# Performance work log

Measured on AMD Instinct MI355X. Metric: run time of the kernel, lower is better.

## Reference

```python
import jax, jax.numpy as jnp
import numpy as np

HEADS = 12
EPS = 1e-5

def setup_inputs() -> dict:
    key = jax.random.key(0)
    ks = jax.random.split(key, 24)
    B, T, H = 128, 128, 768
    RIN, RH, NT = 512, 512, 10
    s = 0.02
    inp = {
        'slot_vector': jax.random.normal(ks[0], (B, H), jnp.float32),
        'utt_vectors': jax.random.normal(ks[1], (B, T, H), jnp.float32),
        'Wq': jax.random.normal(ks[2], (H, H), jnp.float32) * s,
        'bq': jnp.zeros((H,), jnp.float32),
        'Wk': jax.random.normal(ks[3], (H, H), jnp.float32) * s,
        'bk': jnp.zeros((H,), jnp.float32),
        'Wv': jax.random.normal(ks[4], (H, H), jnp.float32) * s,
        'bv': jnp.zeros((H,), jnp.float32),
        'Wo': jax.random.normal(ks[5], (H, H), jnp.float32) * s,
        'bo': jnp.zeros((H,), jnp.float32),
        'W_in': jax.random.normal(ks[6], (RIN, 2 * H), jnp.float32) * s,
        'b_in': jnp.zeros((RIN,), jnp.float32),
        'W_ih': jax.random.normal(ks[7], (4 * RH, RIN), jnp.float32) * s,
        'W_hh': jax.random.normal(ks[8], (4 * RH, RH), jnp.float32) * s,
        'b_ih': jnp.zeros((4 * RH,), jnp.float32),
        'b_hh': jnp.zeros((4 * RH,), jnp.float32),
        'W_tag': jax.random.normal(ks[9], (NT, RH), jnp.float32) * s,
        'b_tag': jnp.zeros((NT,), jnp.float32),
        'ln_g': jnp.ones((NT,), jnp.float32),
        'ln_b': jnp.zeros((NT,), jnp.float32),
    }
    return inp

def _forward(slot_vector, utt_vectors, Wq, bq, Wk, bk, Wv, bv, Wo, bo,
             W_in, b_in, W_ih, W_hh, b_ih, b_hh, W_tag, b_tag, ln_g, ln_b):
    B, T, H = utt_vectors.shape
    dk = H // HEADS
    # Multi-head attention: Q is slot vector (seq len 1), K/V are utt encodings
    q = (slot_vector @ Wq.T + bq).reshape(B, 1, HEADS, dk).transpose(0, 2, 1, 3)  # [B,h,1,dk]
    k = (utt_vectors @ Wk.T + bk).reshape(B, T, HEADS, dk).transpose(0, 2, 1, 3)  # [B,h,T,dk]
    v = (utt_vectors @ Wv.T + bv).reshape(B, T, HEADS, dk).transpose(0, 2, 1, 3)
    scores = jnp.einsum('bhqd,bhkd->bhqk', q, k) / jnp.sqrt(jnp.float32(dk))
    attn = jax.nn.softmax(scores, axis=-1)
    X = jnp.einsum('bhqk,bhkd->bhqd', attn, v).transpose(0, 2, 1, 3).reshape(B, H)
    X = X @ Wo.T + bo  # [B, H] context vector, fixed across timesteps
    RH = W_hh.shape[1]
    h0 = jnp.zeros((B, RH), jnp.float32)
    c0 = jnp.zeros((B, RH), jnp.float32)

    def step(carry, x_t):
        h, c = carry
        lstm_in = jax.nn.sigmoid(jnp.concatenate([x_t, X], axis=1) @ W_in.T + b_in)
        gates = lstm_in @ W_ih.T + b_ih + h @ W_hh.T + b_hh  # [B, 4*RH]
        i_g, f_g, g_g, o_g = jnp.split(gates, 4, axis=1)  # torch gate order i,f,g,o
        c = jax.nn.sigmoid(f_g) * c + jax.nn.sigmoid(i_g) * jnp.tanh(g_g)
        h = jax.nn.sigmoid(o_g) * jnp.tanh(c)
        y = h @ W_tag.T + b_tag  # [B, NT]
        mu = jnp.mean(y, axis=-1, keepdims=True)
        var = jnp.mean((y - mu) ** 2, axis=-1, keepdims=True)
        y = (y - mu) / jnp.sqrt(var + EPS) * ln_g + ln_b
        return (h, c), y

    xs = utt_vectors.transpose(1, 0, 2)  # [T, B, H]
    _, ys = jax.lax.scan(step, (h0, c0), xs)  # ys: [T, B, NT]
    return ys.transpose(1, 2, 0)  # [B, NT, T]

def reference(slot_vector, utt_vectors, Wq, bq, Wk, bk, Wv, bv, Wo, bo,
              W_in, b_in, W_ih, W_hh, b_ih, b_hh, W_tag, b_tag, ln_g, ln_b):
    return _forward(slot_vector, utt_vectors, Wq, bq, Wk, bk, Wv, bv, Wo, bo,
                    W_in, b_in, W_ih, W_hh, b_ih, b_hh, W_tag, b_tag, ln_g, ln_b)
```

## Files before the change

kernel.cpp:

```cpp
#include <hip/hip_runtime.h>
#include <hip/hip_bf16.h>
#include <math.h>

#define Bc 128
#define Tc 128
#define Hc 768
#define NHEAD 12
#define DKc 64
#define RHc 512
#define G4c 2048
#define NTc 10
#define LNEPS 1e-5f
#define NSLC 16

typedef short bf16x8 __attribute__((ext_vector_type(8)));
typedef float f32x4 __attribute__((ext_vector_type(4)));

__device__ __forceinline__ float sigmoidf_(float x) { return 1.0f / (1.0f + __expf(-x)); }

__device__ __forceinline__ ushort f2bf(float f) {
  union { float f; uint u; } c; c.f = f;
  uint r = (c.u + 0x7FFFu + ((c.u >> 16) & 1u)) >> 16;
  return (ushort)r;
}
__device__ __forceinline__ float bf2f(ushort u) {
  union { uint u; float f; } c; c.u = ((uint)u) << 16;
  return c.f;
}
__device__ __forceinline__ uint pack2(float a, float b) {
  return (uint)f2bf(a) | ((uint)f2bf(b) << 16);
}

__global__ void bias_sum_perm_k(const float* __restrict__ a, const float* __restrict__ b,
                                float* __restrict__ o) {
  int i = blockIdx.x * blockDim.x + threadIdx.x;
  if (i < G4c) {
    const int g = i >> 9, u = i & 511;
    o[u * 4 + g] = a[i] + b[i];
  }
}

__global__ void cvt4_k(const float* __restrict__ x, ushort* __restrict__ y, int n4) {
  int i = blockIdx.x * 256 + threadIdx.x;
  if (i < n4) {
    float4 v = ((const float4*)x)[i];
    ushort4 o; o.x = f2bf(v.x); o.y = f2bf(v.y); o.z = f2bf(v.z); o.w = f2bf(v.w);
    ((ushort4*)y)[i] = o;
  }
}

__global__ __launch_bounds__(256) void cvt_wih_perm_k(
    const float* __restrict__ W, ushort* __restrict__ out)
{
  const int rp = blockIdx.x;
  const int u = rp >> 2, g = rp & 3;
  const float* src = W + (size_t)(g * 512 + u) * 512;
  ushort* dst = out + (size_t)rp * 512;
  for (int k = threadIdx.x; k < 512; k += 256) dst[k] = f2bf(src[k]);
}

__global__ __launch_bounds__(256) void cvt_whh_frag_k(
    const float* __restrict__ Whh, ushort* __restrict__ out)
{
  const int idx = blockIdx.x * 256 + threadIdx.x;
  const int lane = idx & 63;
  const int kf = (idx >> 6) & 15;
  const int sw = idx >> 10;
  const int m = lane & 15;
  const int u = (sw >> 3) * 32 + (sw & 7) * 4 + (m >> 2);
  const int gate = m & 3;
  const int k0 = kf * 32 + (lane >> 4) * 8;
  const float* src = Whh + ((size_t)(gate * RHc + u)) * RHc + k0;
  ushort4 o0, o1;
  o0.x = f2bf(src[0]); o0.y = f2bf(src[1]); o0.z = f2bf(src[2]); o0.w = f2bf(src[3]);
  o1.x = f2bf(src[4]); o1.y = f2bf(src[5]); o1.z = f2bf(src[6]); o1.w = f2bf(src[7]);
  ushort* dst = out + (size_t)idx * 8;
  *(ushort4*)dst = o0;
  *(ushort4*)(dst + 4) = o1;
}

__global__ __launch_bounds__(256) void bgemm_bt(
    const void* __restrict__ Aptr, const ushort* __restrict__ Wb,
    const float* __restrict__ bias, void* __restrict__ Cptr,
    int M, int N, int K, int amode, int outMode,
    const float* __restrict__ utt, const float* __restrict__ xo, int trow0)
{
  __shared__ ushort As[128 * 40];
  __shared__ ushort Ws[128 * 40];
  const int tid = threadIdx.x;
  const int lane = tid & 63, wid = tid >> 6;
  const int wm = wid >> 1, wn = wid & 1;
  const int row0 = blockIdx.y * 128, col0 = blockIdx.x * 128;

  f32x4 acc[4][4];
#pragma unroll
  for (int i = 0; i < 4; ++i)
#pragma unroll
    for (int j = 0; j < 4; ++j) {
      f32x4 z = {0.f, 0.f, 0.f, 0.f};
      acc[i][j] = z;
    }

  const int r = tid >> 1, kq = (tid & 1) * 16;

  for (int kb = 0; kb < K; kb += 32) {
    const int k = kb + kq;
    if (amode == 2) {
      const ushort* ap = (const ushort*)Aptr + (size_t)(row0 + r) * K + k;
      *(uint4*)&As[r * 40 + kq] = *(const uint4*)ap;
      *(uint4*)&As[r * 40 + kq + 8] = *(const uint4*)(ap + 8);
    } else {
      const float* ap;
      if (amode == 0) {
        ap = (const float*)Aptr + (size_t)(row0 + r) * K + k;
      } else {
        const int b = r;
        const int t = trow0 + blockIdx.y;
        ap = (k < Hc) ? utt + ((size_t)b * Tc + t) * Hc + k
                      : xo + (size_t)b * Hc + (k - Hc);
      }
      const float4 f0 = *(const float4*)ap;
      const float4 f1 = *(const float4*)(ap + 4);
      const float4 f2 = *(const float4*)(ap + 8);
      const float4 f3 = *(const float4*)(ap + 12);
      uint4 u0, u1;
      u0.x = pack2(f0.x, f0.y); u0.y = pack2(f0.z, f0.w);
      u0.z = pack2(f1.x, f1.y); u0.w = pack2(f1.z, f1.w);
      u1.x = pack2(f2.x, f2.y); u1.y = pack2(f2.z, f2.w);
      u1.z = pack2(f3.x, f3.y); u1.w = pack2(f3.z, f3.w);
      *(uint4*)&As[r * 40 + kq] = u0;
      *(uint4*)&As[r * 40 + kq + 8] = u1;
    }
    {
      const ushort* wp = Wb + (size_t)(col0 + r) * K + k;
      *(uint4*)&Ws[r * 40 + kq] = *(const uint4*)wp;
      *(uint4*)&Ws[r * 40 + kq + 8] = *(const uint4*)(wp + 8);
    }
    __syncthreads();
    const int koff = (lane >> 4) * 8;
    const int ar = wm * 64 + (lane & 15);
    const int wr = wn * 64 + (lane & 15);
    bf16x8 af[4], wf[4];
#pragma unroll
    for (int i = 0; i < 4; ++i) af[i] = *(const bf16x8*)&As[(ar + i * 16) * 40 + koff];
#pragma unroll
    for (int i = 0; i < 4; ++i) wf[i] = *(const bf16x8*)&Ws[(wr + i * 16) * 40 + koff];
#pragma unroll
    for (int fm = 0; fm < 4; ++fm)
#pragma unroll
      for (int fn = 0; fn < 4; ++fn)
        acc[fm][fn] = __builtin_amdgcn_mfma_f32_16x16x32_bf16(af[fm], wf[fn], acc[fm][fn], 0, 0, 0);
    __syncthreads();
  }

#pragma unroll
  for (int fm = 0; fm < 4; ++fm) {
    const int m0 = row0 + wm * 64 + fm * 16 + ((lane >> 4) * 4);
#pragma unroll
    for (int fn = 0; fn < 4; ++fn) {
      const int n = col0 + wn * 64 + fn * 16 + (lane & 15);
      const float bb = bias[n];
#pragma unroll
      for (int q = 0; q < 4; ++q) {
        const float v = acc[fm][fn][q] + bb;
        if (outMode == 1)
          ((ushort*)Cptr)[(size_t)(m0 + q) * N + n] = f2bf(sigmoidf_(v));
        else
          ((float*)Cptr)[(size_t)(m0 + q) * N + n] = v;
      }
    }
  }
}

__global__ __launch_bounds__(256) void fold_qp_k(
    const float* __restrict__ slot, const float* __restrict__ Wq,
    const float* __restrict__ bq, const float* __restrict__ Wk,
    const float* __restrict__ bk, ushort* __restrict__ Pb, float* __restrict__ cqB)
{
  __shared__ float ss[Hc];
  __shared__ float qp[4][DKc];
  __shared__ float qs[DKc];
  const int bx = blockIdx.x;
  const int b = bx / NHEAD, h = bx % NHEAD;
  const int tid = threadIdx.x;
  for (int i = tid; i < Hc; i += 256) ss[i] = slot[(size_t)b * Hc + i];
  __syncthreads();
  {
    const int d = tid & 63, qt = tid >> 6;
    const float* wr = Wq + (size_t)(h * DKc + d) * Hc + qt * 192;
    const float* sb = ss + qt * 192;
    float a = 0.f;
    for (int e = 0; e < 192; e += 4) {
      const float4 wv = *(const float4*)(wr + e);
      a += wv.x * sb[e] + wv.y * sb[e + 1] + wv.z * sb[e + 2] + wv.w * sb[e + 3];
    }
    qp[qt][d] = a;
  }
  __syncthreads();
  if (tid < DKc)
    qs[tid] = qp[0][tid] + qp[1][tid] + qp[2][tid] + qp[3][tid] + bq[h * DKc + tid];
  __syncthreads();
  if (tid < DKc) {
    float pv = qs[tid] * bk[h * DKc + tid];
#pragma unroll
    for (int off = 32; off; off >>= 1) pv += __shfl_xor(pv, off);
    if (tid == 0) cqB[b * NHEAD + h] = pv;
  }
  for (int j = tid; j < Hc; j += 256) {
    float a = 0.f;
#pragma unroll 8
    for (int d = 0; d < DKc; ++d)
      a = fmaf(qs[d], Wk[(size_t)(h * DKc + d) * Hc + j], a);
    Pb[((size_t)b * NHEAD + h) * Hc + j] = f2bf(a);
  }
}

__global__ __launch_bounds__(256) void attn_scores2_k(
    const ushort* __restrict__ Pb, const float* __restrict__ cqB,
    const float* __restrict__ utt, float* __restrict__ Att)
{
  __shared__ float Phs[NHEAD][Hc];
  __shared__ float sc[NHEAD][Tc];
  const int b = blockIdx.x;
  const int tid = threadIdx.x;
  for (int i = tid; i < NHEAD * Hc; i += 256)
    ((float*)Phs)[i] = bf2f(Pb[(size_t)b * NHEAD * Hc + i]);
  __syncthreads();
  const int t = tid & 127, hh = tid >> 7;
  const int h0 = hh * 6;
  float a6[6];
#pragma unroll
  for (int i = 0; i < 6; ++i) a6[i] = 0.f;
  const float* xr = utt + ((size_t)b * Tc + t) * Hc;
  for (int j = 0; j < Hc; j += 4) {
    const float4 xv = *(const float4*)(xr + j);
#pragma unroll
    for (int i = 0; i < 6; ++i) {
      a6[i] = fmaf(xv.x, Phs[h0 + i][j], a6[i]);
      a6[i] = fmaf(xv.y, Phs[h0 + i][j + 1], a6[i]);
      a6[i] = fmaf(xv.z, Phs[h0 + i][j + 2], a6[i]);
      a6[i] = fmaf(xv.w, Phs[h0 + i][j + 3], a6[i]);
    }
  }
#pragma unroll
  for (int i = 0; i < 6; ++i)
    sc[h0 + i][t] = (a6[i] + cqB[b * NHEAD + h0 + i]) * 0.125f;
  __syncthreads();
  const int w = tid >> 6, lane = tid & 63;
#pragma unroll
  for (int i = 0; i < 3; ++i) {
    const int h = w * 3 + i;
    const float s0 = sc[h][lane], s1 = sc[h][lane + 64];
    float m = fmaxf(s0, s1);
#pragma unroll
    for (int off = 32; off; off >>= 1) m = fmaxf(m, __shfl_xor(m, off));
    const float e0 = expf(s0 - m), e1 = expf(s1 - m);
    float s = e0 + e1;
#pragma unroll
    for (int off = 32; off; off >>= 1) s += __shfl_xor(s, off);
    const float inv = 1.f / s;
    Att[((size_t)b * NHEAD + h) * Tc + lane] = e0 * inv;
    Att[((size_t)b * NHEAD + h) * Tc + lane + 64] = e1 * inv;
  }
}

__global__ __launch_bounds__(256) void attn_uxc_k(
    const float* __restrict__ Att, const float* __restrict__ utt,
    const float* __restrict__ Wv, const float* __restrict__ bv,
    float* __restrict__ Xc)
{
  __shared__ float As[NHEAD][Tc];
  __shared__ float Us[NHEAD * Hc];
  const int b = blockIdx.x;
  const int tid = threadIdx.x;
  for (int i = tid; i < NHEAD * Tc; i += 256)
    ((float*)As)[i] = Att[(size_t)b * NHEAD * Tc + i];
  __syncthreads();
  float acc[NHEAD][3];
#pragma unroll
  for (int h = 0; h < NHEAD; ++h)
#pragma unroll
    for (int q = 0; q < 3; ++q) acc[h][q] = 0.f;
  for (int t = 0; t < Tc; ++t) {
    const float* xr = utt + ((size_t)b * Tc + t) * Hc;
    const float x0 = xr[tid], x1 = xr[tid + 256], x2 = xr[tid + 512];
#pragma unroll
    for (int h = 0; h < NHEAD; ++h) {
      const float a = As[h][t];
      acc[h][0] = fmaf(a, x0, acc[h][0]);
      acc[h][1] = fmaf(a, x1, acc[h][1]);
      acc[h][2] = fmaf(a, x2, acc[h][2]);
    }
  }
#pragma unroll
  for (int h = 0; h < NHEAD; ++h)
#pragma unroll
    for (int q = 0; q < 3; ++q)
      Us[h * Hc + tid + q * 256] = acc[h][q];
  __syncthreads();
#pragma unroll
  for (int rr = 0; rr < 3; ++rr) {
    const int hd = tid + rr * 256;
    const int h = hd >> 6;
    const float* wr = Wv + (size_t)hd * Hc;
    const float* ub = Us + h * Hc;
    float a = 0.f;
    for (int j = 0; j < Hc; j += 4) {
      const float4 w4 = *(const float4*)(wr + j);
      a += w4.x * ub[j] + w4.y * ub[j + 1] + w4.z * ub[j + 2] + w4.w * ub[j + 3];
    }
    Xc[(size_t)b * Hc + hd] = a + bv[hd];
  }
}

__device__ __forceinline__ void group_barrier(unsigned* line) {
  __syncthreads();
  if (threadIdx.x == 0) {
    __builtin_amdgcn_fence(__ATOMIC_RELEASE, "agent");
    unsigned g = __hip_atomic_load(line + 1, __ATOMIC_RELAXED, __HIP_MEMORY_SCOPE_AGENT);
    unsigned a = __hip_atomic_fetch_add(line, 1u, __ATOMIC_ACQ_REL, __HIP_MEMORY_SCOPE_AGENT);
    if (a == NSLC - 1) {
      __hip_atomic_store(line, 0u, __ATOMIC_RELAXED, __HIP_MEMORY_SCOPE_AGENT);
      __hip_atomic_store(line + 1, g + 1u, __ATOMIC_RELEASE, __HIP_MEMORY_SCOPE_AGENT);
    } else {
      while (__hip_atomic_load(line + 1, __ATOMIC_RELAXED, __HIP_MEMORY_SCOPE_AGENT) == g)
        __builtin_amdgcn_s_sleep(1);
      __builtin_amdgcn_fence(__ATOMIC_ACQUIRE, "agent");
    }
  }
  __syncthreads();
}

__global__ __launch_bounds__(512, 1) void lstm_mfma_k(
    const ushort* __restrict__ WhhF, const float* __restrict__ GXc,
    ushort* __restrict__ hbuf, float* __restrict__ Hch,
    float* __restrict__ Cb, int t0, int nsteps, unsigned* __restrict__ bars)
{
  const int blk = blockIdx.x;
  const int gid = blk & 7, sid = blk >> 3;
  const int tid = threadIdx.x;
  const int w = tid >> 6, lane = tid & 63;
  const int bl = lane & 15, uq = lane >> 4;
  const int uglob = sid * 32 + w * 4 + uq;
  const int bglob = gid * 16 + bl;
  unsigned* line = bars + gid * 32;

  bf16x8 afr[16];
  {
    const ushort* base = WhhF + ((size_t)((sid * 8 + w) * 16) * 64 + lane) * 8;
#pragma unroll
    for (int kf = 0; kf < 16; ++kf)
      afr[kf] = *(const bf16x8*)(base + (size_t)kf * 64 * 8);
  }

  float creg = (t0 > 0) ? Cb[(size_t)bglob * RHc + uglob] : 0.f;
  ushort* hbg = hbuf + (size_t)gid * (2 * 16 * RHc);

  float4 gx4 = *(const float4*)(GXc + ((size_t)0 * Bc + bglob) * G4c + uglob * 4);

  for (int s = 0; s < nsteps; ++s) {
    const int t = t0 + s;
    f32x4 acc = {0.f, 0.f, 0.f, 0.f};
    if (t > 0) {
      const ushort* hsrc = hbg + (size_t)((t & 1) ^ 1) * (16 * RHc) + (size_t)bl * RHc + uq * 8;
#pragma unroll
      for (int kf = 0; kf < 16; ++kf) {
        const bf16x8 bf = *(const bf16x8*)(hsrc + kf * 32);
        acc = __builtin_amdgcn_mfma_f32_16x16x32_bf16(afr[kf], bf, acc, 0, 0, 0);
      }
    }
    const float gi = gx4.x + acc[0];
    const float gf = gx4.y + acc[1];
    const float gg = gx4.z + acc[2];
    const float go = gx4.w + acc[3];
    const float iv = sigmoidf_(gi);
    const float fv = sigmoidf_(gf);
    const float gv = tanhf(gg);
    const float ov = sigmoidf_(go);
    creg = fmaf(fv, creg, iv * gv);
    const float hval = ov * tanhf(creg);
    hbg[(size_t)(t & 1) * (16 * RHc) + (size_t)bl * RHc + uglob] = f2bf(hval);
    Hch[((size_t)s * Bc + bglob) * RHc + uglob] = hval;
    if (s != nsteps - 1) {
      gx4 = *(const float4*)(GXc + ((size_t)(s + 1) * Bc + bglob) * G4c + uglob * 4);
      group_barrier(line);
    }
  }
  Cb[(size_t)bglob * RHc + uglob] = creg;
}

__global__ __launch_bounds__(256) void tag_ln_k(
    const float* __restrict__ Hch, const float* __restrict__ Wtag,
    const float* __restrict__ btag, const float* __restrict__ lng,
    const float* __restrict__ lnb, float* __restrict__ out, int t0)
{
  const int wid = (blockIdx.x * blockDim.x + threadIdx.x) >> 6;
  const int lane = threadIdx.x & 63;
  const int tl = wid >> 7, b = wid & 127;
  const int t = t0 + tl;
  const float* hp = Hch + ((size_t)tl * Bc + b) * RHc;
  float y[NTc];
#pragma unroll
  for (int j = 0; j < NTc; ++j) y[j] = 0.f;
  for (int k = lane; k < RHc; k += 64) {
    const float hv = hp[k];
#pragma unroll
    for (int j = 0; j < NTc; ++j)
      y[j] = fmaf(hv, Wtag[(size_t)j * RHc + k], y[j]);
  }
#pragma unroll
  for (int off = 32; off > 0; off >>= 1)
#pragma unroll
    for (int j = 0; j < NTc; ++j)
      y[j] += __shfl_xor(y[j], off);
  float mu = 0.f;
#pragma unroll
  for (int j = 0; j < NTc; ++j) { y[j] += btag[j]; mu += y[j]; }
  mu *= (1.0f / NTc);
  float var = 0.f;
#pragma unroll
  for (int j = 0; j < NTc; ++j) { const float d = y[j] - mu; var = fmaf(d, d, var); }
  var *= (1.0f / NTc);
  const float inv = rsqrtf(var + LNEPS);
  if (lane < NTc) {
    out[(size_t)b * NTc * Tc + (size_t)lane * Tc + t] =
        (y[lane] - mu) * inv * lng[lane] + lnb[lane];
  }
}

extern "C" void kernel_launch(void* const* d_in, const int* in_sizes, int n_in,
                              void* d_out, int out_size, void* d_ws, size_t ws_size,
                              hipStream_t stream)
{
  const float* slot = (const float*)d_in[0];
  const float* utt  = (const float*)d_in[1];
  const float* Wq = (const float*)d_in[2];   const float* bq = (const float*)d_in[3];
  const float* Wk = (const float*)d_in[4];   const float* bk = (const float*)d_in[5];
  const float* Wv = (const float*)d_in[6];   const float* bv = (const float*)d_in[7];
  const float* Wo = (const float*)d_in[8];   const float* bo = (const float*)d_in[9];
  const float* W_in = (const float*)d_in[10]; const float* b_in = (const float*)d_in[11];
  const float* W_ih = (const float*)d_in[12]; const float* W_hh = (const float*)d_in[13];
  const float* b_ih = (const float*)d_in[14]; const float* b_hh = (const float*)d_in[15];
  const float* W_tag = (const float*)d_in[16]; const float* b_tag = (const float*)d_in[17];
  const float* ln_g = (const float*)d_in[18]; const float* ln_b = (const float*)d_in[19];
  float* out = (float*)d_out;
  float* ws = (float*)d_ws;

  int CHT = 16;
  while (CHT > 2 && 4ull * (2265088ull + 360448ull * (unsigned)CHT) > ws_size)
    CHT >>= 1;
  const int NCH = Tc / CHT;

  float* Xc    = ws;
  float* Xo    = Xc + 98304;
  float* bsum  = Xo + 98304;
  float* Cb    = bsum + 2048;
  float* Att   = Cb + 65536;
  ushort* hbuf = (ushort*)(Att + 196608);
  ushort* WinB = (ushort*)(ws + 526336);
  ushort* WihB = (ushort*)(ws + 919552);
  ushort* WoB  = (ushort*)(ws + 1443840);
  ushort* WhhF = (ushort*)(ws + 1738752);
  float* cqB   = ws + 2263040;
  unsigned* bars = (unsigned*)(ws + 2264576);
  ushort* LINc = (ushort*)(ws + 2265088);
  float* GXc   = ws + 2265088 + (size_t)32768 * CHT;
  float* Hch   = GXc + (size_t)262144 * CHT;
  ushort* Pb   = (ushort*)(ws + 2265088);

  (void)hipMemsetAsync(bars, 0, 2048, stream);

  hipLaunchKernelGGL(cvt4_k, dim3(768), dim3(256), 0, stream, W_in, WinB, 196608);
  hipLaunchKernelGGL(cvt_wih_perm_k, dim3(2048), dim3(256), 0, stream, W_ih, WihB);
  hipLaunchKernelGGL(cvt4_k, dim3(576), dim3(256), 0, stream, Wo, WoB, 147456);
  hipLaunchKernelGGL(cvt_whh_frag_k, dim3(512), dim3(256), 0, stream, W_hh, WhhF);
  hipLaunchKernelGGL(bias_sum_perm_k, dim3(8), dim3(256), 0, stream, b_ih, b_hh, bsum);

  hipLaunchKernelGGL(fold_qp_k, dim3(Bc * NHEAD), dim3(256), 0, stream,
                     slot, Wq, bq, Wk, bk, Pb, cqB);
  hipLaunchKernelGGL(attn_scores2_k, dim3(Bc), dim3(256), 0, stream, Pb, cqB, utt, Att);
  hipLaunchKernelGGL(attn_uxc_k, dim3(Bc), dim3(256), 0, stream, Att, utt, Wv, bv, Xc);
  hipLaunchKernelGGL(bgemm_bt, dim3(6, 1), dim3(256), 0, stream,
                     (const void*)Xc, WoB, bo, (void*)Xo, 128, 768, 768, 0, 0,
                     (const float*)nullptr, (const float*)nullptr, 0);

  for (int tc = 0; tc < NCH; ++tc) {
    hipLaunchKernelGGL(bgemm_bt, dim3(4, CHT), dim3(256), 0, stream,
                       (const void*)nullptr, WinB, b_in, (void*)LINc,
                       CHT * Bc, 512, 1536, 1, 1, utt, Xo, tc * CHT);
    hipLaunchKernelGGL(bgemm_bt, dim3(16, CHT), dim3(256), 0, stream,
                       (const void*)LINc, WihB, bsum, (void*)GXc,
                       CHT * Bc, 2048, 512, 2, 0,
                       (const float*)nullptr, (const float*)nullptr, 0);
    hipLaunchKernelGGL(lstm_mfma_k, dim3(128), dim3(512), 0, stream,
                       WhhF, GXc, hbuf, Hch, Cb, tc * CHT, CHT, bars);
    hipLaunchKernelGGL(tag_ln_k, dim3(CHT * 32), dim3(256), 0, stream,
                       Hch, W_tag, b_tag, ln_g, ln_b, out, tc * CHT);
  }
}
```

Before: 2.344 ms.

## Halve LSTM recurrence blocks by giving each wave two unit tiles

The recurrent LSTM kernel now assigns two 16x16 MFMA tiles of W_hh to each wave, so the grid drops from 128 to 64 blocks and each per-group barrier spans 8 instead of 16 blocks. The shared h fragment is loaded once and reused for both MFMA chains, and tanhf is replaced by a cheaper exp-based formula. This is meant to cut grid-barrier synchronization cost and h reloads per step, at the price of doubled per-thread work and register pressure (32 A fragments) and a slightly less accurate tanh.

New measurement: 2.134 ms (median of 2 runs). 1.1x faster.

```diff
diff --git a/kernel.cpp b/kernel.cpp
--- a/kernel.cpp
+++ b/kernel.cpp
@@ -11,12 +11,13 @@
 #define G4c 2048
 #define NTc 10
 #define LNEPS 1e-5f
-#define NSLC 16
+#define NSLC 8
 
 typedef short bf16x8 __attribute__((ext_vector_type(8)));
 typedef float f32x4 __attribute__((ext_vector_type(4)));
 
 __device__ __forceinline__ float sigmoidf_(float x) { return 1.0f / (1.0f + __expf(-x)); }
+__device__ __forceinline__ float tanhf_(float x) { return 1.0f - 2.0f / (__expf(2.0f * x) + 1.0f); }
 
 __device__ __forceinline__ ushort f2bf(float f) {
   union { float f; uint u; } c; c.f = f;
@@ -65,9 +66,9 @@
   const int idx = blockIdx.x * 256 + threadIdx.x;
   const int lane = idx & 63;
   const int kf = (idx >> 6) & 15;
-  const int sw = idx >> 10;
+  const int ti = idx >> 10;
   const int m = lane & 15;
-  const int u = (sw >> 3) * 32 + (sw & 7) * 4 + (m >> 2);
+  const int u = (ti >> 3) * 32 + (ti & 7) * 4 + (m >> 2);
   const int gate = m & 3;
   const int k0 = kf * 32 + (lane >> 4) * 8;
   const float* src = Whh + ((size_t)(gate * RHc + u)) * RHc + k0;
@@ -341,52 +342,76 @@
   const int tid = threadIdx.x;
   const int w = tid >> 6, lane = tid & 63;
   const int bl = lane & 15, uq = lane >> 4;
-  const int uglob = sid * 32 + w * 4 + uq;
   const int bglob = gid * 16 + bl;
   unsigned* line = bars + gid * 32;
 
-  bf16x8 afr[16];
+  const int ti0 = sid * 16 + w * 2;
+  const int ug0 = ((ti0 >> 3) << 5) + ((ti0 & 7) << 2) + uq;
+  const int ti1 = ti0 + 1;
+  const int ug1 = ((ti1 >> 3) << 5) + ((ti1 & 7) << 2) + uq;
+
+  bf16x8 afr0[16], afr1[16];
   {
-    const ushort* base = WhhF + ((size_t)((sid * 8 + w) * 16) * 64 + lane) * 8;
-#pragma unroll
-    for (int kf = 0; kf < 16; ++kf)
-      afr[kf] = *(const bf16x8*)(base + (size_t)kf * 64 * 8);
-  }
-
-  float creg = (t0 > 0) ? Cb[(size_t)bglob * RHc + uglob] : 0.f;
+    const ushort* b0 = WhhF + ((size_t)(ti0 * 16) * 64 + lane) * 8;
+    const ushort* b1 = WhhF + ((size_t)(ti1 * 16) * 64 + lane) * 8;
+#pragma unroll
+    for (int kf = 0; kf < 16; ++kf) {
+      afr0[kf] = *(const bf16x8*)(b0 + (size_t)kf * 512);
+      afr1[kf] = *(const bf16x8*)(b1 + (size_t)kf * 512);
+    }
+  }
+
+  float c0 = 0.f, c1 = 0.f;
+  if (t0 > 0) {
+    c0 = Cb[(size_t)bglob * RHc + ug0];
+    c1 = Cb[(size_t)bglob * RHc + ug1];
+  }
   ushort* hbg = hbuf + (size_t)gid * (2 * 16 * RHc);
 
-  float4 gx4 = *(const float4*)(GXc + ((size_t)0 * Bc + bglob) * G4c + uglob * 4);
+  float4 gxa = *(const float4*)(GXc + ((size_t)0 * Bc + bglob) * G4c + ug0 * 4);
+  float4 gxb = *(const float4*)(GXc + ((size_t)0 * Bc + bglob) * G4c + ug1 * 4);
 
   for (int s = 0; s < nsteps; ++s) {
     const int t = t0 + s;
-    f32x4 acc = {0.f, 0.f, 0.f, 0.f};
+    f32x4 acc0 = {0.f, 0.f, 0.f, 0.f};
+    f32x4 acc1 = {0.f, 0.f, 0.f, 0.f};
     if (t > 0) {
       const ushort* hsrc = hbg + (size_t)((t & 1) ^ 1) * (16 * RHc) + (size_t)bl * RHc + uq * 8;
 #pragma unroll
       for (int kf = 0; kf < 16; ++kf) {
         const bf16x8 bf = *(const bf16x8*)(hsrc + kf * 32);
-        acc = __builtin_amdgcn_mfma_f32_16x16x32_bf16(afr[kf], bf, acc, 0, 0, 0);
+        acc0 = __builtin_amdgcn_mfma_f32_16x16x32_bf16(afr0[kf], bf, acc0, 0, 0, 0);
+        acc1 = __builtin_amdgcn_mfma_f32_16x16x32_bf16(afr1[kf], bf, acc1, 0, 0, 0);
       }
     }
-    const float gi = gx4.x + acc[0];
-    const float gf = gx4.y + acc[1];
-    const float gg = gx4.z + acc[2];
-    const float go = gx4.w + acc[3];
-    const float iv = sigmoidf_(gi);
-    const float fv = sigmoidf_(gf);
-    const float gv = tanhf(gg);
-    const float ov = sigmoidf_(go);
-    creg = fmaf(fv, creg, iv * gv);
-    const float hval = ov * tanhf(creg);
-    hbg[(size_t)(t & 1) * (16 * RHc) + (size_t)bl * RHc + uglob] = f2bf(hval);
-    Hch[((size_t)s * Bc + bglob) * RHc + uglob] = hval;
+    {
+      const float iv = sigmoidf_(gxa.x + acc0[0]);
+      const float fv = sigmoidf_(gxa.y + acc0[1]);
+      const float gv = tanhf_(gxa.z + acc0[2]);
+      const float ov = sigmoidf_(gxa.w + acc0[3]);
+      c0 = fmaf(fv, c0, iv * gv);
+      const float hval = ov * tanhf_(c0);
+      hbg[(size_t)(t & 1) * (16 * RHc) + (size_t)bl * RHc + ug0] = f2bf(hval);
+      Hch[((size_t)s * Bc + bglob) * RHc + ug0] = hval;
+    }
+    {
+      const float iv = sigmoidf_(gxb.x + acc1[0]);
+      const float fv = sigmoidf_(gxb.y + acc1[1]);
+      const float gv = tanhf_(gxb.z + acc1[2]);
+      const float ov = sigmoidf_(gxb.w + acc1[3]);
+      c1 = fmaf(fv, c1, iv * gv);
+      const float hval = ov * tanhf_(c1);
+      hbg[(size_t)(t & 1) * (16 * RHc) + (size_t)bl * RHc + ug1] = f2bf(hval);
+      Hch[((size_t)s * Bc + bglob) * RHc + ug1] = hval;
+    }
     if (s != nsteps - 1) {
-      gx4 = *(const float4*)(GXc + ((size_t)(s + 1) * Bc + bglob) * G4c + uglob * 4);
+      gxa = *(const float4*)(GXc + ((size_t)(s + 1) * Bc + bglob) * G4c + ug0 * 4);
+      gxb = *(const float4*)(GXc + ((size_t)(s + 1) * Bc + bglob) * G4c + ug1 * 4);
       group_barrier(line);
     }
   }
-  Cb[(size_t)bglob * RHc + uglob] = creg;
+  Cb[(size_t)bglob * RHc + ug0] = c0;
+  Cb[(size_t)bglob * RHc + ug1] = c1;
 }
 
 __global__ __launch_bounds__(256) void tag_ln_k(
@@ -492,7 +517,7 @@
                        (const void*)LINc, WihB, bsum, (void*)GXc,
                        CHT * Bc, 2048, 512, 2, 0,
                        (const float*)nullptr, (const float*)nullptr, 0);
-    hipLaunchKernelGGL(lstm_mfma_k, dim3(128), dim3(512), 0, stream,
+    hipLaunchKernelGGL(lstm_mfma_k, dim3(64), dim3(512), 0, stream,
                        WhhF, GXc, hbuf, Hch, Cb, tc * CHT, CHT, bars);
     hipLaunchKernelGGL(tag_ln_k, dim3(CHT * 32), dim3(256), 0, stream,
                        Hch, W_tag, b_tag, ln_g, ln_b, out, tc * CHT);
```
